# Kernel tuning notes

Hardware: AMD Instinct MI355X
Metric: run time of the kernel (lower is better)

## Reference

```python
import math
import jax, jax.numpy as jnp
import numpy as np

B, L, D, H, NL, BS = 4, 1024, 512, 8, 6, 1024
HS = D // H  # 64
NUM_STAGES, STAGE_DIM = 32, 8
NUM_CHARS, CHAR_DIM = 32, 16
NUM_ACTIONS, ACT_DIM = 512, 32
GS_DIM, CTRL_DIM = 64, 32
IN_SIZE = STAGE_DIM + 2 * CHAR_DIM + 2 * ACT_DIM + GS_DIM + CTRL_DIM  # 200
C_OUT, M_OUT, B_OUT, S_OUT = 21, 21, 12, 4
C_IN, M_IN = D, D + C_OUT
B_IN, S_IN = M_IN + M_OUT, M_IN + M_OUT + B_OUT


def _ln(x, w, b):
    mu = jnp.mean(x, -1, keepdims=True)
    var = jnp.mean(jnp.square(x - mu), -1, keepdims=True)
    return (x - mu) * jax.lax.rsqrt(var + 1e-5) * w + b


def _skew(QEr):
    # Music-Transformer skew trick: pad col, reshape, drop first row.
    b, h, r, c = QEr.shape
    padded = jnp.pad(QEr, ((0, 0), (0, 0), (0, 0), (1, 0)))
    return padded.reshape(b, h, c + 1, r)[:, :, 1:, :]


def _head(x, lnw, lnb, W1, b1, W2, b2):
    h = _ln(x, lnw, lnb)
    return jax.nn.gelu(h @ W1 + b1, approximate=False) @ W2 + b2


def _forward(stage, egoc, oppc, egoa, oppa,
             gamestate, controller, emb_stage, emb_char, emb_action,
             Wd, bd, ln1w, ln1b, Wqkv, bqkv, Wo, bo, Er,
             ln2w, ln2b, Wfc, bfc, Wp, bp, lnfw, lnfb,
             hc_lnw, hc_lnb, hc_W1, hc_b1, hc_W2, hc_b2,
             hm_lnw, hm_lnb, hm_W1, hm_b1, hm_W2, hm_b2,
             hb_lnw, hb_lnb, hb_W1, hb_b1, hb_W2, hb_b2,
             hs_lnw, hs_lnb, hs_W1, hs_b1, hs_W2, hs_b2):
    sg = jax.lax.stop_gradient
    x = jnp.concatenate([
        emb_stage[stage[..., 0]], emb_char[egoc[..., 0]], emb_char[oppc[..., 0]],
        emb_action[egoa[..., 0]], emb_action[oppa[..., 0]], gamestate, controller], -1)
    x = x @ Wd + bd  # [B, L, D]
    Ls = x.shape[1]
    mask = jnp.tril(jnp.ones((Ls, Ls), dtype=bool))
    scale = 1.0 / math.sqrt(HS)
    for i in range(NL):
        h = _ln(x, ln1w[i], ln1b[i])
        qkv = h @ Wqkv[i] + bqkv[i]
        q, k, v = jnp.split(qkv, 3, axis=-1)
        q = q.reshape(B, Ls, H, HS).transpose(0, 2, 1, 3)
        k = k.reshape(B, Ls, H, HS).transpose(0, 2, 1, 3)
        v = v.reshape(B, Ls, H, HS).transpose(0, 2, 1, 3)
        QEr = jnp.einsum('bhld,md->bhlm', q, Er[i][BS - Ls:, :])
        att = (jnp.einsum('bhld,bhmd->bhlm', q, k) + _skew(QEr)) * scale
        att = jnp.where(mask, att, -jnp.inf)
        att = jax.nn.softmax(att, axis=-1)
        y = jnp.einsum('bhlm,bhmd->bhld', att, v).transpose(0, 2, 1, 3).reshape(B, Ls, D)
        x = x + y @ Wo[i] + bo[i]
        h2 = _ln(x, ln2w[i], ln2b[i])
        x = x + jax.nn.gelu(h2 @ Wfc[i] + bfc[i], approximate=False) @ Wp[i] + bp[i]
    x = _ln(x, lnfw, lnfb)
    c = _head(x, hc_lnw, hc_lnb, hc_W1, hc_b1, hc_W2, hc_b2)
    m = _head(jnp.concatenate([x, sg(c)], -1), hm_lnw, hm_lnb, hm_W1, hm_b1, hm_W2, hm_b2)
    bt = _head(jnp.concatenate([x, sg(c), sg(m)], -1), hb_lnw, hb_lnb, hb_W1, hb_b1, hb_W2, hb_b2)
    s = _head(jnp.concatenate([x, sg(c), sg(m), sg(bt)], -1), hs_lnw, hs_lnb, hs_W1, hs_b1, hs_W2, hs_b2)
    return jnp.concatenate([c, m, bt, s], -1)  # [B, L, 58]


def setup_inputs() -> dict:
    key = jax.random.key(0)
    ki = iter(jax.random.split(key, 64))
    def nrm(shape, s=0.02):
        return (jax.random.normal(next(ki), shape) * s).astype(jnp.float32)
    z = lambda *shape: jnp.zeros(shape, jnp.float32)
    o = lambda *shape: jnp.ones(shape, jnp.float32)
    proj_std = 0.02 / math.sqrt(2 * NL)
    inp = {}
    inp['stage'] = jax.random.randint(next(ki), (B, L, 1), 0, NUM_STAGES, dtype=jnp.int32)
    inp['ego_character'] = jax.random.randint(next(ki), (B, L, 1), 0, NUM_CHARS, dtype=jnp.int32)
    inp['opponent_character'] = jax.random.randint(next(ki), (B, L, 1), 0, NUM_CHARS, dtype=jnp.int32)
    inp['ego_action'] = jax.random.randint(next(ki), (B, L, 1), 0, NUM_ACTIONS, dtype=jnp.int32)
    inp['opponent_action'] = jax.random.randint(next(ki), (B, L, 1), 0, NUM_ACTIONS, dtype=jnp.int32)
    inp['gamestate'] = jax.random.normal(next(ki), (B, L, GS_DIM), dtype=jnp.float32)
    inp['controller'] = jax.random.normal(next(ki), (B, L, CTRL_DIM), dtype=jnp.float32)
    inp['emb_stage'] = nrm((NUM_STAGES, STAGE_DIM))
    inp['emb_char'] = nrm((NUM_CHARS, CHAR_DIM))
    inp['emb_action'] = nrm((NUM_ACTIONS, ACT_DIM))
    inp['Wd'] = nrm((IN_SIZE, D)); inp['bd'] = z(D)
    inp['ln1w'] = o(NL, D); inp['ln1b'] = z(NL, D)
    inp['Wqkv'] = nrm((NL, D, 3 * D)); inp['bqkv'] = z(NL, 3 * D)
    inp['Wo'] = nrm((NL, D, D), proj_std); inp['bo'] = z(NL, D)
    inp['Er'] = jax.random.normal(next(ki), (NL, BS, HS), dtype=jnp.float32)
    inp['ln2w'] = o(NL, D); inp['ln2b'] = z(NL, D)
    inp['Wfc'] = nrm((NL, D, 4 * D)); inp['bfc'] = z(NL, 4 * D)
    inp['Wp'] = nrm((NL, 4 * D, D), proj_std); inp['bp'] = z(NL, D)
    inp['lnfw'] = o(D); inp['lnfb'] = z(D)
    for pre, d_in, d_out in [('hc', C_IN, C_OUT), ('hm', M_IN, M_OUT), ('hb', B_IN, B_OUT), ('hs', S_IN, S_OUT)]:
        d_h = d_in // 2
        inp[pre + '_lnw'] = o(d_in); inp[pre + '_lnb'] = z(d_in)
        inp[pre + '_W1'] = nrm((d_in, d_h)); inp[pre + '_b1'] = z(d_h)
        inp[pre + '_W2'] = nrm((d_h, d_out)); inp[pre + '_b2'] = z(d_out)
    return inp


def reference(stage, ego_character, opponent_character, ego_action, opponent_action,
              gamestate, controller, emb_stage, emb_char, emb_action,
              Wd, bd, ln1w, ln1b, Wqkv, bqkv, Wo, bo, Er,
              ln2w, ln2b, Wfc, bfc, Wp, bp, lnfw, lnfb,
              hc_lnw, hc_lnb, hc_W1, hc_b1, hc_W2, hc_b2,
              hm_lnw, hm_lnb, hm_W1, hm_b1, hm_W2, hm_b2,
              hb_lnw, hb_lnb, hb_W1, hb_b1, hb_W2, hb_b2,
              hs_lnw, hs_lnb, hs_W1, hs_b1, hs_W2, hs_b2):
    return _forward(stage, ego_character, opponent_character, ego_action, opponent_action,
                    gamestate, controller, emb_stage, emb_char, emb_action,
                    Wd, bd, ln1w, ln1b, Wqkv, bqkv, Wo, bo, Er,
                    ln2w, ln2b, Wfc, bfc, Wp, bp, lnfw, lnfb,
                    hc_lnw, hc_lnb, hc_W1, hc_b1, hc_W2, hc_b2,
                    hm_lnw, hm_lnb, hm_W1, hm_b1, hm_W2, hm_b2,
                    hb_lnw, hb_lnb, hb_W1, hb_b1, hb_W2, hb_b2,
                    hs_lnw, hs_lnb, hs_W1, hs_b1, hs_W2, hs_b2)
```

## Files before the change

### kernel.cpp

```cpp
#include <hip/hip_runtime.h>
#include <math.h>

typedef unsigned short u16;
typedef __bf16 bf16x8 __attribute__((ext_vector_type(8)));
typedef short s16x8 __attribute__((ext_vector_type(8)));
typedef short s16x4 __attribute__((ext_vector_type(4)));
typedef float f32x4 __attribute__((ext_vector_type(4)));

__device__ __forceinline__ u16 f2b(float f) {
  union { float f; unsigned u; } x; x.f = f;
  unsigned r = x.u + 0x7fff + ((x.u >> 16) & 1);
  return (u16)(r >> 16);
}

__device__ __forceinline__ void gload16(const void* g, void* l) {
  __builtin_amdgcn_global_load_lds((const __attribute__((address_space(1))) unsigned int*)g,
                                   (__attribute__((address_space(3))) unsigned int*)l, 16, 0, 0);
}

__global__ void embed_kernel(const int* __restrict__ stage, const int* __restrict__ egoc,
                             const int* __restrict__ oppc, const int* __restrict__ egoa,
                             const int* __restrict__ oppa,
                             const float* __restrict__ gamestate, const float* __restrict__ controller,
                             const float* __restrict__ emb_stage, const float* __restrict__ emb_char,
                             const float* __restrict__ emb_action,
                             u16* __restrict__ xinb) {
  int t = blockIdx.x;
  int c = threadIdx.x;
  if (c >= 224) return;
  float v = 0.f;
  if (c < 8)        v = emb_stage[stage[t] * 8 + c];
  else if (c < 24)  v = emb_char[egoc[t] * 16 + (c - 8)];
  else if (c < 40)  v = emb_char[oppc[t] * 16 + (c - 24)];
  else if (c < 72)  v = emb_action[egoa[t] * 32 + (c - 40)];
  else if (c < 104) v = emb_action[oppa[t] * 32 + (c - 72)];
  else if (c < 168) v = gamestate[t * 64 + (c - 104)];
  else if (c < 200) v = controller[t * 32 + (c - 168)];
  xinb[t * 224 + c] = f2b(v);
}

template<typename T>
__global__ void ln_kernel(const float* __restrict__ in, int ldi,
                          T* __restrict__ out, int ldo,
                          const float* __restrict__ w, const float* __restrict__ b,
                          int d, int dpad) {
  int wid = threadIdx.x >> 6;
  int lane = threadIdx.x & 63;
  int row = blockIdx.x * 4 + wid;
  const float* ip = in + (size_t)row * ldi;
  float v[9];
  int n = 0;
  float s = 0.f;
  for (int c = lane; c < d; c += 64) { v[n] = ip[c]; s += v[n]; n++; }
  #pragma unroll
  for (int o = 32; o; o >>= 1) s += __shfl_xor(s, o);
  float mu = s / (float)d;
  float q = 0.f;
  for (int i = 0; i < n; i++) { float t = v[i] - mu; q += t * t; }
  #pragma unroll
  for (int o = 32; o; o >>= 1) q += __shfl_xor(q, o);
  float rstd = rsqrtf(q / (float)d + 1e-5f);
  T* op = out + (size_t)row * ldo;
  int c = lane;
  for (int i = 0; i < n; i++, c += 64) {
    float val = (v[i] - mu) * rstd * w[c] + b[c];
    if constexpr (sizeof(T) == 2) op[c] = f2b(val); else op[c] = val;
  }
  for (int cz = (d & ~63) + lane; cz < dpad; cz += 64)
    if (cz >= d) { if constexpr (sizeof(T) == 2) op[cz] = 0; else op[cz] = 0.f; }
}

__global__ void ln512_kernel(const float* __restrict__ in, u16* __restrict__ out,
                             const float* __restrict__ w, const float* __restrict__ b) {
  int wid = threadIdx.x >> 6, lane = threadIdx.x & 63;
  int row = blockIdx.x * 4 + wid;
  const float4* ip = (const float4*)(in + (size_t)row * 512);
  float4 x0 = ip[lane], x1 = ip[lane + 64];
  float s = x0.x + x0.y + x0.z + x0.w + x1.x + x1.y + x1.z + x1.w;
  #pragma unroll
  for (int o = 32; o; o >>= 1) s += __shfl_xor(s, o);
  float mu = s * (1.f / 512.f);
  float q = (x0.x-mu)*(x0.x-mu) + (x0.y-mu)*(x0.y-mu) + (x0.z-mu)*(x0.z-mu) + (x0.w-mu)*(x0.w-mu)
          + (x1.x-mu)*(x1.x-mu) + (x1.y-mu)*(x1.y-mu) + (x1.z-mu)*(x1.z-mu) + (x1.w-mu)*(x1.w-mu);
  #pragma unroll
  for (int o = 32; o; o >>= 1) q += __shfl_xor(q, o);
  float rstd = rsqrtf(q * (1.f / 512.f) + 1e-5f);
  const float4* w4 = (const float4*)w;
  const float4* b4 = (const float4*)b;
  float4 w0 = w4[lane], w1 = w4[lane + 64], c0 = b4[lane], c1 = b4[lane + 64];
  ushort4 o0, o1;
  o0.x = f2b((x0.x - mu) * rstd * w0.x + c0.x);
  o0.y = f2b((x0.y - mu) * rstd * w0.y + c0.y);
  o0.z = f2b((x0.z - mu) * rstd * w0.z + c0.z);
  o0.w = f2b((x0.w - mu) * rstd * w0.w + c0.w);
  o1.x = f2b((x1.x - mu) * rstd * w1.x + c1.x);
  o1.y = f2b((x1.y - mu) * rstd * w1.y + c1.y);
  o1.z = f2b((x1.z - mu) * rstd * w1.z + c1.z);
  o1.w = f2b((x1.w - mu) * rstd * w1.w + c1.w);
  *(ushort4*)(out + (size_t)row * 512 + lane * 4) = o0;
  *(ushort4*)(out + (size_t)row * 512 + 256 + lane * 4) = o1;
}

struct TJob { const float* src; u16* dst; int K, N, Kout, Nout, start; };
struct TJobs { TJob j[26]; int njobs; };

__global__ void multi_tpose(TJobs jobs) {
  int bid = blockIdx.x;
  int ji = 0;
  while (ji + 1 < jobs.njobs && bid >= jobs.j[ji + 1].start) ji++;
  TJob jb = jobs.j[ji];
  int local = bid - jb.start;
  int ntx = jb.Nout >> 5;
  int n0 = (local % ntx) << 5;
  int k0 = (local / ntx) << 5;
  __shared__ float tile[32][33];
  int tx = threadIdx.x & 31, ty = threadIdx.x >> 5;
  #pragma unroll
  for (int q = 0; q < 4; q++) {
    int k = k0 + ty + q * 8, n = n0 + tx;
    tile[ty + q * 8][tx] = (k < jb.K && n < jb.N) ? jb.src[(size_t)k * jb.N + n] : 0.f;
  }
  __syncthreads();
  #pragma unroll
  for (int q = 0; q < 4; q++)
    jb.dst[(size_t)(n0 + ty + q * 8) * jb.Kout + k0 + tx] = f2b(tile[tx][ty + q * 8]);
}

__global__ void b16conv_kernel(const float* __restrict__ in, u16* __restrict__ out, int n) {
  int i = blockIdx.x * 256 + threadIdx.x;
  if (i < n) out[i] = f2b(in[i]);
}

struct PBias { const float* b1[4]; const float* b2[4]; int dh[4]; int dout[4]; };
__global__ void pad_bias_kernel(PBias pb, float* __restrict__ b1p, float* __restrict__ b2p) {
  int t = threadIdx.x;
  for (int hd = 0; hd < 4; hd++) {
    for (int c = t; c < 288; c += 256) b1p[hd * 288 + c] = (c < pb.dh[hd]) ? pb.b1[hd][c] : 0.f;
    for (int c = t; c < 64; c += 256)  b2p[hd * 64 + c] = (c < pb.dout[hd]) ? pb.b2[hd][c] : 0.f;
  }
}

template<int BN>
__global__ __launch_bounds__(256, 2) void mgemm_kernel(
    const u16* __restrict__ A, const u16* __restrict__ Bt, const float* __restrict__ bias,
    float* __restrict__ Cf, u16* __restrict__ Cb, int K, int ldc, int flags, int Nreal,
    float* __restrict__ Cf2, int coff2) {
  constexpr int NR = BN / 32;
  __shared__ u16 As[2][128 * 32];
  __shared__ u16 Bs[2][BN * 32];
  const int t = threadIdx.x;
  const int row0 = blockIdx.y * 128;
  const int col0 = blockIdx.x * BN;
  const int lane = t & 63, wv = t >> 6;
  const int wr = wv >> 1, wc = wv & 1;
  const int lr = lane & 15, lk = lane >> 4;

  f32x4 acc[4][NR];
  #pragma unroll
  for (int m = 0; m < 4; m++)
    #pragma unroll
    for (int n = 0; n < NR; n++) acc[m][n] = (f32x4){0.f, 0.f, 0.f, 0.f};

  auto stage = [&](int buf, int kt) {
    #pragma unroll
    for (int r = 0; r < 2; r++) {
      int c = t + 256 * r;
      gload16(A + (size_t)(row0 + (c >> 2)) * K + kt + (c & 3) * 8, &As[buf][c * 8]);
    }
    for (int c = t; c < BN * 4; c += 256)
      gload16(Bt + (size_t)(col0 + (c >> 2)) * K + kt + (c & 3) * 8, &Bs[buf][c * 8]);
  };

  stage(0, 0);
  const int nt = K >> 5;
  const int abase = (wr * 64 + lr) * 32 + lk * 8;
  const int bbase = (wc * (BN / 2) + lr) * 32 + lk * 8;
  for (int tile = 0; tile < nt; tile++) {
    __syncthreads();
    int cur = tile & 1;
    if (tile + 1 < nt) stage(cur ^ 1, (tile + 1) * 32);
    bf16x8 af[4], bfr[NR];
    #pragma unroll
    for (int m = 0; m < 4; m++) af[m] = *(const bf16x8*)&As[cur][abase + m * 16 * 32];
    #pragma unroll
    for (int n = 0; n < NR; n++) bfr[n] = *(const bf16x8*)&Bs[cur][bbase + n * 16 * 32];
    #pragma unroll
    for (int m = 0; m < 4; m++)
      #pragma unroll
      for (int n = 0; n < NR; n++)
        acc[m][n] = __builtin_amdgcn_mfma_f32_16x16x32_bf16(af[m], bfr[n], acc[m][n], 0, 0, 0);
  }
  #pragma unroll
  for (int m = 0; m < 4; m++) {
    int row = row0 + wr * 64 + m * 16 + lk * 4;
    #pragma unroll
    for (int n = 0; n < NR; n++) {
      int col = col0 + wc * (BN / 2) + n * 16 + lr;
      if (col >= Nreal) continue;
      float bc = bias[col];
      #pragma unroll
      for (int r = 0; r < 4; r++) {
        float v = acc[m][n][r] + bc;
        if (flags & 2) v = 0.5f * v * (1.f + erff(v * 0.70710678118f));
        size_t idx = (size_t)(row + r) * ldc + col;
        if (flags & 1) Cf[idx] += v;
        if (flags & 4) Cf[idx] = v;
        if (flags & 8) Cb[idx] = f2b(v);
        if (flags & 16) Cf2[(size_t)(row + r) * 58 + col + coff2] = v;
      }
    }
  }
}

__global__ __launch_bounds__(256, 3) void attn_kernel(
    const u16* __restrict__ qkv,
    const u16* __restrict__ Erb,
    u16* __restrict__ y) {
  __shared__ u16 Qs[64 * 72];
  __shared__ u16 Ks[64 * 72];
  __shared__ u16 Vt[64 * 72];
  __shared__ u16 Es[128 * 72];
  u16* const Ps = Qs;

  const int qi = (int)gridDim.x - 1 - (int)blockIdx.x;
  const int L0 = qi * 64;
  const int h = blockIdx.y, b = blockIdx.z;
  const int t = threadIdx.x, lane = t & 63, w = t >> 6;
  const int lr = lane & 15, lk = lane >> 4;
  const size_t base = (size_t)b * 1024 * 1536;

  #pragma unroll
  for (int r = 0; r < 2; r++) {
    int c = t + 256 * r;
    int qr = c >> 3, ko = c & 7;
    s16x8 v = *(const s16x8*)(qkv + base + (size_t)(L0 + qr) * 1536 + h * 64 + ko * 8);
    *(s16x8*)&Qs[qr * 72 + ko * 8] = v;
  }
  __syncthreads();
  const bf16x8 aq0 = *(const bf16x8*)&Qs[(w * 16 + lr) * 72 + lk * 8];
  const bf16x8 aq1 = *(const bf16x8*)&Qs[(w * 16 + lr) * 72 + lk * 8 + 32];

  const int jr0 = t >> 3, ko0 = t & 7;
  const int jr1 = jr0 + 32;
  const int vswz = (jr0 >> 3) ^ ko0;
  s16x8 kpre[2], vpre[2];
  const u16* const kgb = qkv + base + 512 + h * 64 + ko0 * 8;
  const u16* const vgb = qkv + base + 1024 + h * 64 + ko0 * 8;
  auto prefetch = [&](int j0) {
    kpre[0] = *(const s16x8*)(kgb + (size_t)(j0 + jr0) * 1536);
    kpre[1] = *(const s16x8*)(kgb + (size_t)(j0 + jr1) * 1536);
    vpre[0] = *(const s16x8*)(vgb + (size_t)(j0 + jr0) * 1536);
    vpre[1] = *(const s16x8*)(vgb + (size_t)(j0 + jr1) * 1536);
  };
  prefetch(0);

  f32x4 acc_o[4];
  float mrow[4], srow[4];
  #pragma unroll
  for (int n = 0; n < 4; n++) acc_o[n] = (f32x4){0.f, 0.f, 0.f, 0.f};
  #pragma unroll
  for (int r = 0; r < 4; r++) { mrow[r] = -INFINITY; srow[r] = 0.f; }

  const int lq0 = L0 + w * 16;
  const int ntiles = qi + 1;
  const f32x4 z4 = (f32x4){0.f, 0.f, 0.f, 0.f};

  for (int tt = 0; tt < ntiles; tt++) {
    const int j0 = tt * 64;
    __syncthreads();
    *(s16x8*)&Ks[jr0 * 72 + ko0 * 8] = kpre[0];
    *(s16x8*)&Ks[jr1 * 72 + ko0 * 8] = kpre[1];
    #pragma unroll
    for (int q = 0; q < 8; q++) {
      int d = ko0 * 8 + q;
      Vt[d * 72 + ((vswz & 7) << 3) + (jr0 & 7)] = (u16)vpre[0][q];
      Vt[d * 72 + (((vswz ^ 4) & 7) << 3) + (jr0 & 7)] = (u16)vpre[1][q];
    }
    const int rb0 = 960 - L0 + j0;
    #pragma unroll
    for (int r = 0; r < 4; r++) {
      int c = t + 256 * r;
      int rb = rb0 + (c >> 3);
      s16x8 ev = {0, 0, 0, 0, 0, 0, 0, 0};
      if (rb < 1024) ev = *(const s16x8*)(Erb + (size_t)rb * 64 + (c & 7) * 8);
      *(s16x8*)&Es[(c >> 3) * 72 + (c & 7) * 8] = ev;
    }
    if (tt + 1 < ntiles) prefetch(j0 + 64);
    __syncthreads();

    f32x4 sacc[4], gacc[5];
    #pragma unroll
    for (int n = 0; n < 4; n++) {
      bf16x8 b0 = *(const bf16x8*)&Ks[(n * 16 + lr) * 72 + lk * 8];
      bf16x8 b1 = *(const bf16x8*)&Ks[(n * 16 + lr) * 72 + lk * 8 + 32];
      sacc[n] = __builtin_amdgcn_mfma_f32_16x16x32_bf16(aq0, b0, z4, 0, 0, 0);
      sacc[n] = __builtin_amdgcn_mfma_f32_16x16x32_bf16(aq1, b1, sacc[n], 0, 0, 0);
    }
    #pragma unroll
    for (int g = 0; g < 5; g++) {
      int er = 48 - 16 * w + g * 16 + lr;
      bf16x8 b0 = *(const bf16x8*)&Es[er * 72 + lk * 8];
      bf16x8 b1 = *(const bf16x8*)&Es[er * 72 + lk * 8 + 32];
      gacc[g] = __builtin_amdgcn_mfma_f32_16x16x32_bf16(aq0, b0, z4, 0, 0, 0);
      gacc[g] = __builtin_amdgcn_mfma_f32_16x16x32_bf16(aq1, b1, gacc[g], 0, 0, 0);
    }

    const bool tile_masked = (j0 + 63 > lq0);
    float pv[4][4], corr[4];
    #pragma unroll
    for (int reg = 0; reg < 4; reg++) {
      int s = 15 - (lk * 4 + reg) + lr;
      int srcl = (lane & 48) | (s & 15);
      int gadd = s >> 4;
      float sh[5];
      #pragma unroll
      for (int g = 0; g < 5; g++) sh[g] = __shfl(gacc[g][reg], srcl, 64);
      int l_abs = lq0 + lk * 4 + reg;
      float sv[4];
      #pragma unroll
      for (int n = 0; n < 4; n++) {
        float gv = gadd ? sh[n + 1] : sh[n];
        float x = (sacc[n][reg] + gv) * 0.125f;
        int j_abs = j0 + n * 16 + lr;
        sv[n] = (tile_masked && j_abs > l_abs) ? -3.0e38f : x;
      }
      float mx = fmaxf(fmaxf(sv[0], sv[1]), fmaxf(sv[2], sv[3]));
      #pragma unroll
      for (int o = 1; o < 16; o <<= 1) mx = fmaxf(mx, __shfl_xor(mx, o, 64));
      float mnew = fmaxf(mrow[reg], mx);
      float cr = __expf(mrow[reg] - mnew);
      mrow[reg] = mnew;
      corr[reg] = cr;
      float ps = 0.f;
      #pragma unroll
      for (int n = 0; n < 4; n++) { float p = __expf(sv[n] - mnew); pv[reg][n] = p; ps += p; }
      #pragma unroll
      for (int o = 1; o < 16; o <<= 1) ps += __shfl_xor(ps, o, 64);
      srow[reg] = srow[reg] * cr + ps;
    }
    #pragma unroll
    for (int reg = 0; reg < 4; reg++) {
      int prow = w * 16 + lk * 4 + reg;
      #pragma unroll
      for (int n = 0; n < 4; n++) Ps[prow * 68 + n * 16 + lr] = f2b(pv[reg][n]);
    }
    #pragma unroll
    for (int n = 0; n < 4; n++) {
      f32x4 o = acc_o[n];
      #pragma unroll
      for (int reg = 0; reg < 4; reg++) o[reg] *= corr[reg];
      acc_o[n] = o;
    }
    union UPS { s16x4 h[2]; bf16x8 v; };
    const int pb = (w * 16 + lr) * 68 + lk * 8;
    UPS u0, u1;
    u0.h[0] = *(const s16x4*)&Ps[pb];
    u0.h[1] = *(const s16x4*)&Ps[pb + 4];
    u1.h[0] = *(const s16x4*)&Ps[pb + 32];
    u1.h[1] = *(const s16x4*)&Ps[pb + 36];
    #pragma unroll
    for (int n = 0; n < 4; n++) {
      int dv = n * 16 + lr;
      int bs = (dv >> 3) & 7;
      bf16x8 b0 = *(const bf16x8*)&Vt[dv * 72 + ((lk ^ bs) << 3)];
      bf16x8 b1 = *(const bf16x8*)&Vt[dv * 72 + ((((lk + 4) ^ bs) & 7) << 3)];
      acc_o[n] = __builtin_amdgcn_mfma_f32_16x16x32_bf16(u0.v, b0, acc_o[n], 0, 0, 0);
      acc_o[n] = __builtin_amdgcn_mfma_f32_16x16x32_bf16(u1.v, b1, acc_o[n], 0, 0, 0);
    }
  }
  #pragma unroll
  for (int reg = 0; reg < 4; reg++) {
    float inv = 1.0f / srow[reg];
    int row = b * 1024 + lq0 + lk * 4 + reg;
    #pragma unroll
    for (int n = 0; n < 4; n++)
      y[(size_t)row * 512 + h * 64 + n * 16 + lr] = f2b(acc_o[n][reg] * inv);
  }
}

extern "C" void kernel_launch(void* const* d_in, const int* in_sizes, int n_in,
                              void* d_out, int out_size, void* d_ws, size_t ws_size,
                              hipStream_t stream) {
  const int* stage = (const int*)d_in[0];
  const int* egoc  = (const int*)d_in[1];
  const int* oppc  = (const int*)d_in[2];
  const int* egoa  = (const int*)d_in[3];
  const int* oppa  = (const int*)d_in[4];
  const float* gamestate  = (const float*)d_in[5];
  const float* controller = (const float*)d_in[6];
  const float* emb_stage  = (const float*)d_in[7];
  const float* emb_char   = (const float*)d_in[8];
  const float* emb_action = (const float*)d_in[9];
  const float* Wd = (const float*)d_in[10];
  const float* bd = (const float*)d_in[11];
  const float* ln1w = (const float*)d_in[12];
  const float* ln1b = (const float*)d_in[13];
  const float* Wqkv = (const float*)d_in[14];
  const float* bqkv = (const float*)d_in[15];
  const float* Wo = (const float*)d_in[16];
  const float* bo = (const float*)d_in[17];
  const float* Er = (const float*)d_in[18];
  const float* ln2w = (const float*)d_in[19];
  const float* ln2b = (const float*)d_in[20];
  const float* Wfc = (const float*)d_in[21];
  const float* bfc = (const float*)d_in[22];
  const float* Wp = (const float*)d_in[23];
  const float* bp = (const float*)d_in[24];
  const float* lnfw = (const float*)d_in[25];
  const float* lnfb = (const float*)d_in[26];

  char* wsb = (char*)d_ws;
  float* x    = (float*)(wsb + 0);
  float* xcat = (float*)(wsb + 8388608);
  u16* hb     = (u16*)(wsb + 17825792);
  u16* qkvb   = (u16*)(wsb + 22020096);
  u16* yb     = (u16*)(wsb + 34603008);
  u16* ffb    = (u16*)(wsb + 38797312);
  u16* erb    = (u16*)(wsb + 55574528);
  u16* wt1    = (u16*)(wsb + 56360960);
  u16* wt2    = (u16*)(wsb + 57933824);
  u16* wt3    = (u16*)(wsb + 58458112);
  u16* wt4    = (u16*)(wsb + 60555264);
  u16* wdt    = (u16*)(wsb + 62652416);
  u16* w1t    = (u16*)(wsb + 62881792);
  u16* w2t    = (u16*)(wsb + 64208896);
  float* b1p  = (float*)(wsb + 64356352);
  float* b2p  = (float*)(wsb + 64360960);
  u16* wall   = (u16*)(wsb + 64365056);
  u16* xinb   = ffb;
  u16* hlnb   = qkvb;
  u16* hhb    = yb;
  float* out  = (float*)d_out;

  const size_t LSTR = 3145728;
  const bool big = ws_size >= (size_t)(64365056 + 6 * LSTR * 2);

  const float* hp[24];
  for (int k = 0; k < 24; k++) hp[k] = (const float*)d_in[27 + k];
  const int din[4]  = {512, 533, 554, 566};
  const int dh[4]   = {256, 266, 277, 283};
  const int dout[4] = {21, 21, 12, 4};

  auto addJob = [](TJobs& J, const float* src, u16* dst, int K, int N, int Kout, int Nout) {
    int i = J.njobs;
    J.j[i].src = src; J.j[i].dst = dst;
    J.j[i].K = K; J.j[i].N = N; J.j[i].Kout = Kout; J.j[i].Nout = Nout;
    J.j[i].start = (i == 0) ? 0
                 : J.j[i - 1].start + (J.j[i - 1].Nout >> 5) * (J.j[i - 1].Kout >> 5);
    J.njobs = i + 1;
  };
  auto jblocks = [](const TJobs& J) {
    const TJob& l = J.j[J.njobs - 1];
    return l.start + (l.Nout >> 5) * (l.Kout >> 5);
  };

  embed_kernel<<<4096, 256, 0, stream>>>(stage, egoc, oppc, egoa, oppa, gamestate,
                                         controller, emb_stage, emb_char, emb_action, xinb);
  b16conv_kernel<<<1536, 256, 0, stream>>>(Er, erb, 6 * 1024 * 64);
  {
    TJobs J; J.njobs = 0;
    addJob(J, Wd, wdt, 200, 512, 224, 512);
    for (int hd = 0; hd < 4; hd++)
      addJob(J, hp[hd * 6 + 2], w1t + hd * 288 * 576, din[hd], dh[hd], 576, 288);
    for (int hd = 0; hd < 4; hd++)
      addJob(J, hp[hd * 6 + 4], w2t + hd * 64 * 288, dh[hd], dout[hd], 288, 64);
    multi_tpose<<<jblocks(J), 256, 0, stream>>>(J);
  }
  if (big) {
    TJobs J; J.njobs = 0;
    for (int i = 0; i < 6; i++) {
      addJob(J, Wqkv + (size_t)i * 512 * 1536, wall + i * LSTR,           512, 1536, 512, 1536);
      addJob(J, Wo   + (size_t)i * 512 * 512,  wall + i * LSTR + 786432,  512, 512,  512, 512);
      addJob(J, Wfc  + (size_t)i * 512 * 2048, wall + i * LSTR + 1048576, 512, 2048, 512, 2048);
      addJob(J, Wp   + (size_t)i * 2048 * 512, wall + i * LSTR + 2097152, 2048, 512, 2048, 512);
    }
    multi_tpose<<<jblocks(J), 256, 0, stream>>>(J);
  }
  {
    PBias pb;
    for (int hd = 0; hd < 4; hd++) {
      pb.b1[hd] = hp[hd * 6 + 3]; pb.b2[hd] = hp[hd * 6 + 5];
      pb.dh[hd] = dh[hd]; pb.dout[hd] = dout[hd];
    }
    pad_bias_kernel<<<1, 256, 0, stream>>>(pb, b1p, b2p);
  }
  mgemm_kernel<128><<<dim3(4, 32), 256, 0, stream>>>(xinb, wdt, bd, x, nullptr,
                                                     224, 512, 4, 1 << 30, nullptr, 0);

  for (int i = 0; i < 6; i++) {
    const u16 *W1p, *W2p, *W3p, *W4p;
    if (big) {
      W1p = wall + i * LSTR;
      W2p = wall + i * LSTR + 786432;
      W3p = wall + i * LSTR + 1048576;
      W4p = wall + i * LSTR + 2097152;
    } else {
      TJobs J; J.njobs = 0;
      addJob(J, Wqkv + (size_t)i * 512 * 1536, wt1, 512, 1536, 512, 1536);
      addJob(J, Wo + (size_t)i * 512 * 512, wt2, 512, 512, 512, 512);
      addJob(J, Wfc + (size_t)i * 512 * 2048, wt3, 512, 2048, 512, 2048);
      addJob(J, Wp + (size_t)i * 2048 * 512, wt4, 2048, 512, 2048, 512);
      multi_tpose<<<jblocks(J), 256, 0, stream>>>(J);
      W1p = wt1; W2p = wt2; W3p = wt3; W4p = wt4;
    }
    ln512_kernel<<<1024, 256, 0, stream>>>(x, hb, ln1w + i * 512, ln1b + i * 512);
    mgemm_kernel<128><<<dim3(12, 32), 256, 0, stream>>>(hb, W1p, bqkv + i * 1536,
                                                        nullptr, qkvb, 512, 1536, 8, 1 << 30, nullptr, 0);
    attn_kernel<<<dim3(16, 8, 4), 256, 0, stream>>>(qkvb, erb + (size_t)i * 1024 * 64, yb);
    mgemm_kernel<64><<<dim3(8, 32), 256, 0, stream>>>(yb, W2p, bo + i * 512,
                                                      x, nullptr, 512, 512, 1, 1 << 30, nullptr, 0);
    ln512_kernel<<<1024, 256, 0, stream>>>(x, hb, ln2w + i * 512, ln2b + i * 512);
    mgemm_kernel<128><<<dim3(16, 32), 256, 0, stream>>>(hb, W3p, bfc + i * 2048,
                                                        nullptr, ffb, 512, 2048, 2 | 8, 1 << 30, nullptr, 0);
    mgemm_kernel<64><<<dim3(8, 32), 256, 0, stream>>>(ffb, W4p, bp + i * 512,
                                                      x, nullptr, 2048, 512, 1, 1 << 30, nullptr, 0);
  }

  ln_kernel<float><<<1024, 256, 0, stream>>>(x, 512, xcat, 576, lnfw, lnfb, 512, 512);
  int col = 512;
  for (int hd = 0; hd < 4; hd++) {
    ln_kernel<u16><<<1024, 256, 0, stream>>>(xcat, 576, hlnb, 576,
                                             hp[hd * 6 + 0], hp[hd * 6 + 1], din[hd], 576);
    mgemm_kernel<96><<<dim3(3, 32), 256, 0, stream>>>(hlnb, w1t + hd * 288 * 576, b1p + hd * 288,
                                                      nullptr, hhb, 576, 288, 2 | 8, 1 << 30, nullptr, 0);
    mgemm_kernel<64><<<dim3(1, 32), 256, 0, stream>>>(hhb, w2t + hd * 64 * 288, b2p + hd * 64,
                                                      xcat + col, nullptr, 288, 576, 4 | 16, dout[hd],
                                                      out, col - 512);
    col += dout[hd];
  }
}
```

Measured before the change: 1.515 ms.

## Split causal attention across KV chunks with merge kernel; shrink GEMM row tiles

Attention now splits each query tile's causal KV range into chunks of 4 tiles. Blocks write partial outputs and running max/sum to workspace, and a new merge kernel combines them with log-sum-exp rescaling. This is meant to fix the load imbalance and low block count of the triangular workload. Separately, the GEMM kernel gains a BM template and all GEMMs use 64-row tiles, doubling the grid to fill more CUs. The cost is extra fp32 partial-result traffic, an extra launch per layer, and lower per-block reuse in the GEMMs.

```diff
diff --git a/kernel.cpp b/kernel.cpp
--- a/kernel.cpp
+++ b/kernel.cpp
@@ -140,61 +140,61 @@
   }
 }
 
-template<int BN>
+template<int BM, int BN>
 __global__ __launch_bounds__(256, 2) void mgemm_kernel(
     const u16* __restrict__ A, const u16* __restrict__ Bt, const float* __restrict__ bias,
     float* __restrict__ Cf, u16* __restrict__ Cb, int K, int ldc, int flags, int Nreal,
     float* __restrict__ Cf2, int coff2) {
-  constexpr int NR = BN / 32;
-  __shared__ u16 As[2][128 * 32];
+  constexpr int NRW = BN / 32;
+  constexpr int MRW = BM / 32;
+  __shared__ u16 As[2][BM * 32];
   __shared__ u16 Bs[2][BN * 32];
   const int t = threadIdx.x;
-  const int row0 = blockIdx.y * 128;
+  const int row0 = blockIdx.y * BM;
   const int col0 = blockIdx.x * BN;
   const int lane = t & 63, wv = t >> 6;
   const int wr = wv >> 1, wc = wv & 1;
   const int lr = lane & 15, lk = lane >> 4;
 
-  f32x4 acc[4][NR];
-  #pragma unroll
-  for (int m = 0; m < 4; m++)
-    #pragma unroll
-    for (int n = 0; n < NR; n++) acc[m][n] = (f32x4){0.f, 0.f, 0.f, 0.f};
+  f32x4 acc[MRW][NRW];
+  #pragma unroll
+  for (int m = 0; m < MRW; m++)
+    #pragma unroll
+    for (int n = 0; n < NRW; n++) acc[m][n] = (f32x4){0.f, 0.f, 0.f, 0.f};
 
   auto stage = [&](int buf, int kt) {
     #pragma unroll
-    for (int r = 0; r < 2; r++) {
-      int c = t + 256 * r;
+    for (int c = t; c < BM * 4; c += 256)
       gload16(A + (size_t)(row0 + (c >> 2)) * K + kt + (c & 3) * 8, &As[buf][c * 8]);
-    }
+    #pragma unroll
     for (int c = t; c < BN * 4; c += 256)
       gload16(Bt + (size_t)(col0 + (c >> 2)) * K + kt + (c & 3) * 8, &Bs[buf][c * 8]);
   };
 
   stage(0, 0);
   const int nt = K >> 5;
-  const int abase = (wr * 64 + lr) * 32 + lk * 8;
+  const int abase = (wr * (BM / 2) + lr) * 32 + lk * 8;
   const int bbase = (wc * (BN / 2) + lr) * 32 + lk * 8;
   for (int tile = 0; tile < nt; tile++) {
     __syncthreads();
     int cur = tile & 1;
     if (tile + 1 < nt) stage(cur ^ 1, (tile + 1) * 32);
-    bf16x8 af[4], bfr[NR];
-    #pragma unroll
-    for (int m = 0; m < 4; m++) af[m] = *(const bf16x8*)&As[cur][abase + m * 16 * 32];
-    #pragma unroll
-    for (int n = 0; n < NR; n++) bfr[n] = *(const bf16x8*)&Bs[cur][bbase + n * 16 * 32];
-    #pragma unroll
-    for (int m = 0; m < 4; m++)
-      #pragma unroll
-      for (int n = 0; n < NR; n++)
+    bf16x8 af[MRW], bfr[NRW];
+    #pragma unroll
+    for (int m = 0; m < MRW; m++) af[m] = *(const bf16x8*)&As[cur][abase + m * 16 * 32];
+    #pragma unroll
+    for (int n = 0; n < NRW; n++) bfr[n] = *(const bf16x8*)&Bs[cur][bbase + n * 16 * 32];
+    #pragma unroll
+    for (int m = 0; m < MRW; m++)
+      #pragma unroll
+      for (int n = 0; n < NRW; n++)
         acc[m][n] = __builtin_amdgcn_mfma_f32_16x16x32_bf16(af[m], bfr[n], acc[m][n], 0, 0, 0);
   }
   #pragma unroll
-  for (int m = 0; m < 4; m++) {
-    int row = row0 + wr * 64 + m * 16 + lk * 4;
-    #pragma unroll
-    for (int n = 0; n < NR; n++) {
+  for (int m = 0; m < MRW; m++) {
+    int row = row0 + wr * (BM / 2) + m * 16 + lk * 4;
+    #pragma unroll
+    for (int n = 0; n < NRW; n++) {
       int col = col0 + wc * (BN / 2) + n * 16 + lr;
       if (col >= Nreal) continue;
       float bc = bias[col];
@@ -212,17 +212,29 @@
   }
 }
 
+template<int CHUNK>
 __global__ __launch_bounds__(256, 3) void attn_kernel(
     const u16* __restrict__ qkv,
     const u16* __restrict__ Erb,
-    u16* __restrict__ y) {
+    u16* __restrict__ y,
+    float* __restrict__ part_o,
+    float* __restrict__ part_ms) {
   __shared__ u16 Qs[64 * 72];
   __shared__ u16 Ks[64 * 72];
   __shared__ u16 Vt[64 * 72];
   __shared__ u16 Es[128 * 72];
   u16* const Ps = Qs;
 
-  const int qi = (int)gridDim.x - 1 - (int)blockIdx.x;
+  int bx = (int)gridDim.x - 1 - (int)blockIdx.x;
+  int g = 0, basep = 0;
+  while (bx >= basep + CHUNK * (g + 1)) { basep += CHUNK * (g + 1); g++; }
+  int off = bx - basep;
+  const int qi = CHUNK * g + off / (g + 1);
+  const int c = off % (g + 1);
+  const int t0 = c * CHUNK;
+  const int t1 = min(t0 + CHUNK, qi + 1);
+  const int nch = qi / CHUNK + 1;
+
   const int L0 = qi * 64;
   const int h = blockIdx.y, b = blockIdx.z;
   const int t = threadIdx.x, lane = t & 63, w = t >> 6;
@@ -231,8 +243,8 @@
 
   #pragma unroll
   for (int r = 0; r < 2; r++) {
-    int c = t + 256 * r;
-    int qr = c >> 3, ko = c & 7;
+    int cc = t + 256 * r;
+    int qr = cc >> 3, ko = cc & 7;
     s16x8 v = *(const s16x8*)(qkv + base + (size_t)(L0 + qr) * 1536 + h * 64 + ko * 8);
     *(s16x8*)&Qs[qr * 72 + ko * 8] = v;
   }
@@ -252,7 +264,7 @@
     vpre[0] = *(const s16x8*)(vgb + (size_t)(j0 + jr0) * 1536);
     vpre[1] = *(const s16x8*)(vgb + (size_t)(j0 + jr1) * 1536);
   };
-  prefetch(0);
+  prefetch(t0 * 64);
 
   f32x4 acc_o[4];
   float mrow[4], srow[4];
@@ -262,10 +274,9 @@
   for (int r = 0; r < 4; r++) { mrow[r] = -INFINITY; srow[r] = 0.f; }
 
   const int lq0 = L0 + w * 16;
-  const int ntiles = qi + 1;
   const f32x4 z4 = (f32x4){0.f, 0.f, 0.f, 0.f};
 
-  for (int tt = 0; tt < ntiles; tt++) {
+  for (int tt = t0; tt < t1; tt++) {
     const int j0 = tt * 64;
     __syncthreads();
     *(s16x8*)&Ks[jr0 * 72 + ko0 * 8] = kpre[0];
@@ -279,13 +290,14 @@
     const int rb0 = 960 - L0 + j0;
     #pragma unroll
     for (int r = 0; r < 4; r++) {
-      int c = t + 256 * r;
-      int rb = rb0 + (c >> 3);
+      int cc = t + 256 * r;
+      int rr = cc >> 3;
+      int rb = rb0 + rr;
       s16x8 ev = {0, 0, 0, 0, 0, 0, 0, 0};
-      if (rb < 1024) ev = *(const s16x8*)(Erb + (size_t)rb * 64 + (c & 7) * 8);
-      *(s16x8*)&Es[(c >> 3) * 72 + (c & 7) * 8] = ev;
-    }
-    if (tt + 1 < ntiles) prefetch(j0 + 64);
+      if (rb < 1024) ev = *(const s16x8*)(Erb + (size_t)rb * 64 + (cc & 7) * 8);
+      *(s16x8*)&Es[rr * 72 + (cc & 7) * 8] = ev;
+    }
+    if (tt + 1 < t1) prefetch(j0 + 64);
     __syncthreads();
 
     f32x4 sacc[4], gacc[5];
@@ -297,12 +309,12 @@
       sacc[n] = __builtin_amdgcn_mfma_f32_16x16x32_bf16(aq1, b1, sacc[n], 0, 0, 0);
     }
     #pragma unroll
-    for (int g = 0; g < 5; g++) {
-      int er = 48 - 16 * w + g * 16 + lr;
+    for (int g2 = 0; g2 < 5; g2++) {
+      int er = 48 - 16 * w + g2 * 16 + lr;
       bf16x8 b0 = *(const bf16x8*)&Es[er * 72 + lk * 8];
       bf16x8 b1 = *(const bf16x8*)&Es[er * 72 + lk * 8 + 32];
-      gacc[g] = __builtin_amdgcn_mfma_f32_16x16x32_bf16(aq0, b0, z4, 0, 0, 0);
-      gacc[g] = __builtin_amdgcn_mfma_f32_16x16x32_bf16(aq1, b1, gacc[g], 0, 0, 0);
+      gacc[g2] = __builtin_amdgcn_mfma_f32_16x16x32_bf16(aq0, b0, z4, 0, 0, 0);
+      gacc[g2] = __builtin_amdgcn_mfma_f32_16x16x32_bf16(aq1, b1, gacc[g2], 0, 0, 0);
     }
 
     const bool tile_masked = (j0 + 63 > lq0);
@@ -314,7 +326,7 @@
       int gadd = s >> 4;
       float sh[5];
       #pragma unroll
-      for (int g = 0; g < 5; g++) sh[g] = __shfl(gacc[g][reg], srcl, 64);
+      for (int g2 = 0; g2 < 5; g2++) sh[g2] = __shfl(gacc[g2][reg], srcl, 64);
       int l_abs = lq0 + lk * 4 + reg;
       float sv[4];
       #pragma unroll
@@ -368,13 +380,73 @@
       acc_o[n] = __builtin_amdgcn_mfma_f32_16x16x32_bf16(u1.v, b1, acc_o[n], 0, 0, 0);
     }
   }
-  #pragma unroll
-  for (int reg = 0; reg < 4; reg++) {
-    float inv = 1.0f / srow[reg];
-    int row = b * 1024 + lq0 + lk * 4 + reg;
-    #pragma unroll
-    for (int n = 0; n < 4; n++)
-      y[(size_t)row * 512 + h * 64 + n * 16 + lr] = f2b(acc_o[n][reg] * inv);
+
+  if (nch == 1) {
+    #pragma unroll
+    for (int reg = 0; reg < 4; reg++) {
+      float inv = 1.0f / srow[reg];
+      int row = b * 1024 + lq0 + lk * 4 + reg;
+      #pragma unroll
+      for (int n = 0; n < 4; n++)
+        y[(size_t)row * 512 + h * 64 + n * 16 + lr] = f2b(acc_o[n][reg] * inv);
+    }
+  } else {
+    const int slot = ((b * 8 + h) * 16 + qi) * 4 + c;
+    #pragma unroll
+    for (int reg = 0; reg < 4; reg++) {
+      int row64 = w * 16 + lk * 4 + reg;
+      if (lr == 0) {
+        part_ms[(size_t)slot * 128 + row64] = mrow[reg];
+        part_ms[(size_t)slot * 128 + 64 + row64] = srow[reg];
+      }
+      #pragma unroll
+      for (int n = 0; n < 4; n++)
+        part_o[(size_t)slot * 4096 + row64 * 64 + n * 16 + lr] = acc_o[n][reg];
+    }
+  }
+}
+
+__global__ void attn_merge(const float* __restrict__ part_o, const float* __restrict__ part_ms,
+                           u16* __restrict__ y) {
+  const int qi = 4 + blockIdx.x;
+  const int h = blockIdx.y, b = blockIdx.z;
+  const int nch = (qi >> 2) + 1;
+  const int row = threadIdx.x >> 2;
+  const int d0 = (threadIdx.x & 3) << 4;
+  const int slotbase = ((b * 8 + h) * 16 + qi) * 4;
+  float m = -INFINITY;
+  for (int cc = 0; cc < nch; cc++)
+    m = fmaxf(m, part_ms[(size_t)(slotbase + cc) * 128 + row]);
+  float s = 0.f;
+  float o[16];
+  #pragma unroll
+  for (int k = 0; k < 16; k++) o[k] = 0.f;
+  for (int cc = 0; cc < nch; cc++) {
+    const size_t sb = (size_t)(slotbase + cc);
+    float mc = part_ms[sb * 128 + row];
+    float sc = part_ms[sb * 128 + 64 + row];
+    float wv = __expf(mc - m);
+    s += sc * wv;
+    const float4* po = (const float4*)(part_o + sb * 4096 + row * 64 + d0);
+    #pragma unroll
+    for (int k4 = 0; k4 < 4; k4++) {
+      float4 v = po[k4];
+      o[k4 * 4 + 0] += v.x * wv;
+      o[k4 * 4 + 1] += v.y * wv;
+      o[k4 * 4 + 2] += v.z * wv;
+      o[k4 * 4 + 3] += v.w * wv;
+    }
+  }
+  float inv = 1.f / s;
+  u16* yp = y + (size_t)(b * 1024 + qi * 64 + row) * 512 + h * 64 + d0;
+  #pragma unroll
+  for (int k4 = 0; k4 < 4; k4++) {
+    ushort4 wv;
+    wv.x = f2b(o[k4 * 4 + 0] * inv);
+    wv.y = f2b(o[k4 * 4 + 1] * inv);
+    wv.z = f2b(o[k4 * 4 + 2] * inv);
+    wv.w = f2b(o[k4 * 4 + 3] * inv);
+    *(ushort4*)(yp + k4 * 4) = wv;
   }
 }
 
@@ -433,7 +505,12 @@
   float* out  = (float*)d_out;
 
   const size_t LSTR = 3145728;
-  const bool big = ws_size >= (size_t)(64365056 + 6 * LSTR * 2);
+  const size_t WALLB = 6 * LSTR * 2;
+  const bool big = ws_size >= (size_t)64365056 + WALLB;
+  const size_t poff = 64365056 + (big ? WALLB : 0);
+  const bool split = ws_size >= poff + 34603008;
+  float* part_o  = (float*)(wsb + poff);
+  float* part_ms = (float*)(wsb + poff + 33554432);
 
   const float* hp[24];
   for (int k = 0; k < 24; k++) hp[k] = (const float*)d_in[27 + k];
@@ -484,8 +561,8 @@
     }
     pad_bias_kernel<<<1, 256, 0, stream>>>(pb, b1p, b2p);
   }
-  mgemm_kernel<128><<<dim3(4, 32), 256, 0, stream>>>(xinb, wdt, bd, x, nullptr,
-                                                     224, 512, 4, 1 << 30, nullptr, 0);
+  mgemm_kernel<64, 64><<<dim3(8, 64), 256, 0, stream>>>(xinb, wdt, bd, x, nullptr,
+                                                        224, 512, 4, 1 << 30, nullptr, 0);
 
   for (int i = 0; i < 6; i++) {
     const u16 *W1p, *W2p, *W3p, *W4p;
@@ -504,16 +581,23 @@
       W1p = wt1; W2p = wt2; W3p = wt3; W4p = wt4;
     }
     ln512_kernel<<<1024, 256, 0, stream>>>(x, hb, ln1w + i * 512, ln1b + i * 512);
-    mgemm_kernel<128><<<dim3(12, 32), 256, 0, stream>>>(hb, W1p, bqkv + i * 1536,
-                                                        nullptr, qkvb, 512, 1536, 8, 1 << 30, nullptr, 0);
-    attn_kernel<<<dim3(16, 8, 4), 256, 0, stream>>>(qkvb, erb + (size_t)i * 1024 * 64, yb);
-    mgemm_kernel<64><<<dim3(8, 32), 256, 0, stream>>>(yb, W2p, bo + i * 512,
-                                                      x, nullptr, 512, 512, 1, 1 << 30, nullptr, 0);
+    mgemm_kernel<64, 128><<<dim3(12, 64), 256, 0, stream>>>(hb, W1p, bqkv + i * 1536,
+                                                            nullptr, qkvb, 512, 1536, 8, 1 << 30, nullptr, 0);
+    if (split) {
+      attn_kernel<4><<<dim3(40, 8, 4), 256, 0, stream>>>(qkvb, erb + (size_t)i * 1024 * 64, yb,
+                                                         part_o, part_ms);
+      attn_merge<<<dim3(12, 8, 4), 256, 0, stream>>>(part_o, part_ms, yb);
+    } else {
+      attn_kernel<16><<<dim3(16, 8, 4), 256, 0, stream>>>(qkvb, erb + (size_t)i * 1024 * 64, yb,
+                                                          x, x);
+    }
+    mgemm_kernel<64, 64><<<dim3(8, 64), 256, 0, stream>>>(yb, W2p, bo + i * 512,
+                                                          x, nullptr, 512, 512, 1, 1 << 30, nullptr, 0);
     ln512_kernel<<<1024, 256, 0, stream>>>(x, hb, ln2w + i * 512, ln2b + i * 512);
-    mgemm_kernel<128><<<dim3(16, 32), 256, 0, stream>>>(hb, W3p, bfc + i * 2048,
-                                                        nullptr, ffb, 512, 2048, 2 | 8, 1 << 30, nullptr, 0);
-    mgemm_kernel<64><<<dim3(8, 32), 256, 0, stream>>>(ffb, W4p, bp + i * 512,
-                                                      x, nullptr, 2048, 512, 1, 1 << 30, nullptr, 0);
+    mgemm_kernel<64, 128><<<dim3(16, 64), 256, 0, stream>>>(hb, W3p, bfc + i * 2048,
+                                                            nullptr, ffb, 512, 2048, 2 | 8, 1 << 30, nullptr, 0);
+    mgemm_kernel<64, 64><<<dim3(8, 64), 256, 0, stream>>>(ffb, W4p, bp + i * 512,
+                                                          x, nullptr, 2048, 512, 1, 1 << 30, nullptr, 0);
   }
 
   ln_kernel<float><<<1024, 256, 0, stream>>>(x, 512, xcat, 576, lnfw, lnfb, 512, 512);
@@ -521,11 +605,11 @@
   for (int hd = 0; hd < 4; hd++) {
     ln_kernel<u16><<<1024, 256, 0, stream>>>(xcat, 576, hlnb, 576,
                                              hp[hd * 6 + 0], hp[hd * 6 + 1], din[hd], 576);
-    mgemm_kernel<96><<<dim3(3, 32), 256, 0, stream>>>(hlnb, w1t + hd * 288 * 576, b1p + hd * 288,
-                                                      nullptr, hhb, 576, 288, 2 | 8, 1 << 30, nullptr, 0);
-    mgemm_kernel<64><<<dim3(1, 32), 256, 0, stream>>>(hhb, w2t + hd * 64 * 288, b2p + hd * 64,
-                                                      xcat + col, nullptr, 288, 576, 4 | 16, dout[hd],
-                                                      out, col - 512);
+    mgemm_kernel<64, 96><<<dim3(3, 64), 256, 0, stream>>>(hlnb, w1t + hd * 288 * 576, b1p + hd * 288,
+                                                          nullptr, hhb, 576, 288, 2 | 8, 1 << 30, nullptr, 0);
+    mgemm_kernel<64, 64><<<dim3(1, 64), 256, 0, stream>>>(hhb, w2t + hd * 64 * 288, b2p + hd * 64,
+                                                          xcat + col, nullptr, 288, 576, 4 | 16, dout[hd],
+                                                          out, col - 512);
     col += dout[hd];
   }
 }
```

Result: faster. 1.238 ms (-18.3%).
